# Kernel optimization log

Hardware: AMD Instinct MI355X
Metric: run time of the kernel (lower is better)

The kernel has to match this reference:

```python
import jax, jax.numpy as jnp
import numpy as np

B = 1 << 21          # shading points per batch
U_RES, CH = 400, 8   # spatial plane
A_RES, ACH = 50, 50 and 8  # placeholder, real consts below
A_RES, ACH = 50, 8   # angular planes (h/d)
HID = 32
IN_CH = CH + 2 * ACH  # 24


def _bilerp_clamp(tex, uv):
    # Bilinear interp, both axes clamped (U-plane). tex: (H,W,C), uv: (B,2) in [0,1]
    H, W, _ = tex.shape
    u = jnp.clip(uv[:, 0], 0.0, 1.0) * (W - 1)
    v = jnp.clip(uv[:, 1], 0.0, 1.0) * (H - 1)
    x0 = jnp.floor(u).astype(jnp.int32)
    x1 = jnp.clip(x0 + 1, 0, W - 1)
    y0 = jnp.floor(v).astype(jnp.int32)
    y1 = jnp.clip(y0 + 1, 0, H - 1)
    ur = (u - x0.astype(u.dtype))[:, None]
    vr = (v - y0.astype(v.dtype))[:, None]
    p00 = tex[y0, x0]; p10 = tex[y0, x1]; p01 = tex[y1, x0]; p11 = tex[y1, x1]
    return ((1 - ur) * (1 - vr) * p00 + ur * (1 - vr) * p10
            + (1 - ur) * vr * p01 + ur * vr * p11)


def _bilerp_wrap_u(tex, uv):
    # Bilinear interp wrapping the u (phi) axis, clamping v (H/D planes).
    H, W, _ = tex.shape
    u = (uv[:, 0] % 1.0) * W
    v = jnp.clip(uv[:, 1], 0.0, 1.0) * (H - 1)
    x0f = jnp.floor(u)
    x0 = x0f.astype(jnp.int32) % W
    x1 = (x0 + 1) % W
    y0 = jnp.floor(v).astype(jnp.int32)
    y1 = jnp.clip(y0 + 1, 0, H - 1)
    ur = (u - x0f)[:, None]
    vr = (v - y0.astype(v.dtype))[:, None]
    p00 = tex[y0, x0]; p10 = tex[y0, x1]; p01 = tex[y1, x0]; p11 = tex[y1, x1]
    return ((1 - ur) * (1 - vr) * p00 + ur * (1 - vr) * p10
            + (1 - ur) * vr * p01 + ur * vr * p11)


def setup_inputs() -> dict:
    key = jax.random.key(0)
    ks = jax.random.split(key, 8)
    x = jax.random.uniform(ks[0], (B, 6), dtype=jnp.float32)
    u_plane = 0.01 * jax.random.normal(ks[1], (U_RES, U_RES, CH), dtype=jnp.float32)
    h_plane = 0.01 * jax.random.normal(ks[2], (A_RES, A_RES, ACH), dtype=jnp.float32)
    d_plane = 0.01 * jax.random.normal(ks[3], (A_RES, A_RES, ACH), dtype=jnp.float32)
    def lin_w(k, fout, fin):  # torch nn.Linear default init (kaiming-uniform-ish)
        lim = 1.0 / np.sqrt(fin)
        return jax.random.uniform(k, (fout, fin), jnp.float32, -lim, lim)
    W0 = lin_w(ks[4], HID, IN_CH)
    W1 = lin_w(ks[5], HID, HID)
    W2 = lin_w(ks[6], HID, HID)
    W3 = lin_w(ks[7], 3, HID)
    return {"x": x, "u_plane": u_plane, "h_plane": h_plane, "d_plane": d_plane,
            "W0": W0, "W1": W1, "W2": W2, "W3": W3}


def reference(x, u_plane, h_plane, d_plane, W0, W1, W2, W3):
    # Split and reorder: H/D planes receive (u=phi, v=theta)
    uv = x[:, 0:2]
    h_uv = jnp.stack((x[:, 3], x[:, 2]), axis=1)
    d_uv = jnp.stack((x[:, 5], x[:, 4]), axis=1)
    fU = _bilerp_clamp(u_plane, uv)       # (B, CH)
    fH = _bilerp_wrap_u(h_plane, h_uv)    # (B, ACH)
    fD = _bilerp_wrap_u(d_plane, d_uv)    # (B, ACH)
    feat = jnp.concatenate([fU, fH, fD], axis=1)  # (B, 24)
    # Quant mode 'off' -> QLinear is a plain bias-free matmul with W^T
    h = jax.nn.relu(feat @ W0.T)
    h = jax.nn.relu(h @ W1.T)
    h = jax.nn.relu(h @ W2.T)
    return h @ W3.T  # (B, 3)
```

## Files before the change

kernel.cpp:

```cpp
#include <hip/hip_runtime.h>

typedef _Float16 half4 __attribute__((ext_vector_type(4)));
typedef _Float16 half8 __attribute__((ext_vector_type(8)));
typedef float floatx4 __attribute__((ext_vector_type(4)));

#define U_RESV 400
#define A_RESV 50

#define UHALVES (U_RESV * U_RESV * 8)
#define AHALVES (A_RESV * A_RESV * 8)
#define WOFF    (UHALVES + 2 * AHALVES)
#define W0OFF   0
#define W1OFF   896
#define W2OFF   2048
#define W3OFF   3200
#define WTOT    3776

__device__ __forceinline__ float clamp01(float x) { return fminf(fmaxf(x, 0.0f), 1.0f); }

__device__ __forceinline__ floatx4 mfma16(half4 a, half4 b, floatx4 c) {
    return __builtin_amdgcn_mfma_f32_16x16x16f16(a, b, c, 0, 0, 0);
}
__device__ __forceinline__ half4 zero4() {
    half4 h; h[0] = h[1] = h[2] = h[3] = (_Float16)0.f; return h;
}
__device__ __forceinline__ half4 relu4(half4 v) {
#if __has_builtin(__builtin_elementwise_max)
    return __builtin_elementwise_max(v, zero4());
#else
    half4 r;
#pragma unroll
    for (int i = 0; i < 4; ++i) r[i] = v[i] > (_Float16)0.f ? v[i] : (_Float16)0.f;
    return r;
#endif
}

__device__ __forceinline__ void cvt_chunk(const float* __restrict__ src,
                                          _Float16* __restrict__ dst, int i) {
    float4 a = *(const float4*)(src + (size_t)i * 8);
    float4 b = *(const float4*)(src + (size_t)i * 8 + 4);
    half8 h;
    h[0] = (_Float16)a.x; h[1] = (_Float16)a.y; h[2] = (_Float16)a.z; h[3] = (_Float16)a.w;
    h[4] = (_Float16)b.x; h[5] = (_Float16)b.y; h[6] = (_Float16)b.z; h[7] = (_Float16)b.w;
    *(half8*)(dst + (size_t)i * 8) = h;
}

__device__ __forceinline__ void wblob_fill(const float* __restrict__ W0,
                                           const float* __restrict__ W1,
                                           const float* __restrict__ W2,
                                           const float* __restrict__ W3,
                                           _Float16* __restrict__ w, int tid, int nthr) {
    for (int i = tid; i < WTOT; i += nthr) {
        float v;
        if (i < W1OFF) {
            int r = i / 28, c = i - r * 28;
            v = (c < 24) ? W0[r * 24 + c] : 0.f;
        } else if (i < W2OFF) {
            int j = i - W1OFF, r = j / 36, c = j - r * 36;
            v = (c < 32) ? W1[r * 32 + c] : 0.f;
        } else if (i < W3OFF) {
            int j = i - W2OFF, r = j / 36, c = j - r * 36;
            v = (c < 32) ? W2[r * 32 + c] : 0.f;
        } else {
            int j = i - W3OFF, r = j / 36, c = j - r * 36;
            v = (r < 3 && c < 32) ? W3[r * 32 + c] : 0.f;
        }
        w[i] = (_Float16)v;
    }
}

__global__ __launch_bounds__(256) void pconv_kernel(
    const float* __restrict__ u_plane, const float* __restrict__ h_plane,
    const float* __restrict__ d_plane, const float* __restrict__ W0,
    const float* __restrict__ W1, const float* __restrict__ W2,
    const float* __restrict__ W3, _Float16* __restrict__ dst) {
    const int gid = blockIdx.x * 256 + threadIdx.x;
    const int gsz = gridDim.x * 256;
    for (int i = gid; i < UHALVES / 8; i += gsz) cvt_chunk(u_plane, dst, i);
    for (int i = gid; i < AHALVES / 8; i += gsz) cvt_chunk(h_plane, dst + UHALVES, i);
    for (int i = gid; i < AHALVES / 8; i += gsz) cvt_chunk(d_plane, dst + UHALVES + AHALVES, i);
    if (blockIdx.x == 0) wblob_fill(W0, W1, W2, W3, dst + WOFF, threadIdx.x, 256);
}

__global__ __launch_bounds__(256) void wprep_kernel(
    const float* __restrict__ W0, const float* __restrict__ W1,
    const float* __restrict__ W2, const float* __restrict__ W3,
    _Float16* __restrict__ wdst) {
    wblob_fill(W0, W1, W2, W3, wdst, threadIdx.x, 256);
}


template <bool F16P>
__global__ __launch_bounds__(512, 2) void tpmlp_kernel(
    const float* __restrict__ x,
    const void* __restrict__ u_tex,
    const void* __restrict__ h_tex,
    const void* __restrict__ d_tex,
    const _Float16* __restrict__ wsw,
    float* __restrict__ out) {
    const int tid  = threadIdx.x;
    const int lane = tid & 63;
    const int wv   = tid >> 6;
    const int q    = lane >> 4;
    const int c15  = lane & 15;

    __shared__ __align__(16) _Float16 fl[512 * 28];
    __shared__ __align__(16) _Float16 wl[WTOT];

    const size_t P = (size_t)blockIdx.x * 512 + tid;
    const float2* xp = (const float2*)(x + P * 6);
    float2 p01v = xp[0], p23v = xp[1], p45v = xp[2];

    uint4 w_a;
    if (tid < 472) w_a = ((const uint4*)wsw)[tid];

    int oU0, oU1, oU2, oU3;  float uw00, uw10, uw01, uw11;
    {
        float u = clamp01(p01v.x) * (float)(U_RESV - 1);
        float v = clamp01(p01v.y) * (float)(U_RESV - 1);
        float x0f = floorf(u), y0f = floorf(v);
        int x0 = (int)x0f, y0 = (int)y0f;
        int x1 = min(x0 + 1, U_RESV - 1), y1 = min(y0 + 1, U_RESV - 1);
        float ur = u - x0f, vr = v - y0f;
        uw00 = (1.0f - ur) * (1.0f - vr); uw10 = ur * (1.0f - vr);
        uw01 = (1.0f - ur) * vr;          uw11 = ur * vr;
        oU0 = (y0 * U_RESV + x0) * 8;
        oU1 = (y0 * U_RESV + x1) * 8;
        oU2 = (y1 * U_RESV + x0) * 8;
        oU3 = (y1 * U_RESV + x1) * 8;
    }
    int oH0, oH1, oH2, oH3;  float hw00, hw10, hw01, hw11;
    {
        float uu = p23v.y, vv = p23v.x;
        float uf = uu - floorf(uu);
        float u = uf * (float)A_RESV;
        float v = clamp01(vv) * (float)(A_RESV - 1);
        float x0f = floorf(u), y0f = floorf(v);
        int x0 = (int)x0f;
        int x1 = x0 + 1; if (x1 == A_RESV) x1 = 0;
        int y0 = (int)y0f;
        int y1 = min(y0 + 1, A_RESV - 1);
        float ur = u - x0f, vr = v - y0f;
        hw00 = (1.0f - ur) * (1.0f - vr); hw10 = ur * (1.0f - vr);
        hw01 = (1.0f - ur) * vr;          hw11 = ur * vr;
        oH0 = (y0 * A_RESV + x0) * 8;
        oH1 = (y0 * A_RESV + x1) * 8;
        oH2 = (y1 * A_RESV + x0) * 8;
        oH3 = (y1 * A_RESV + x1) * 8;
    }
    int oD0, oD1, oD2, oD3;  float dw00, dw10, dw01, dw11;
    {
        float uu = p45v.y, vv = p45v.x;
        float uf = uu - floorf(uu);
        float u = uf * (float)A_RESV;
        float v = clamp01(vv) * (float)(A_RESV - 1);
        float x0f = floorf(u), y0f = floorf(v);
        int x0 = (int)x0f;
        int x1 = x0 + 1; if (x1 == A_RESV) x1 = 0;
        int y0 = (int)y0f;
        int y1 = min(y0 + 1, A_RESV - 1);
        float ur = u - x0f, vr = v - y0f;
        dw00 = (1.0f - ur) * (1.0f - vr); dw10 = ur * (1.0f - vr);
        dw01 = (1.0f - ur) * vr;          dw11 = ur * vr;
        oD0 = (y0 * A_RESV + x0) * 8;
        oD1 = (y0 * A_RESV + x1) * 8;
        oD2 = (y1 * A_RESV + x0) * 8;
        oD3 = (y1 * A_RESV + x1) * 8;
    }

    half8 gU0, gU1, gU2, gU3, gH0, gH1, gH2, gH3, gD0, gD1, gD2, gD3;
    float4 sU0, sU1, sU2, sU3, sH0, sH1, sH2, sH3, sD0, sD1, sD2, sD3;
    float4 rU0, rU1, rU2, rU3, rH0, rH1, rH2, rH3, rD0, rD1, rD2, rD3;
    if constexpr (F16P) {
        const _Float16* up = (const _Float16*)u_tex;
        const _Float16* hp = (const _Float16*)h_tex;
        const _Float16* dp = (const _Float16*)d_tex;
        gU0 = *(const half8*)(up + oU0);
        gU1 = *(const half8*)(up + oU1);
        gU2 = *(const half8*)(up + oU2);
        gU3 = *(const half8*)(up + oU3);
        gH0 = *(const half8*)(hp + oH0);
        gH1 = *(const half8*)(hp + oH1);
        gH2 = *(const half8*)(hp + oH2);
        gH3 = *(const half8*)(hp + oH3);
        gD0 = *(const half8*)(dp + oD0);
        gD1 = *(const half8*)(dp + oD1);
        gD2 = *(const half8*)(dp + oD2);
        gD3 = *(const half8*)(dp + oD3);
    } else {
        const float* up = (const float*)u_tex;
        const float* hp = (const float*)h_tex;
        const float* dp = (const float*)d_tex;
        sU0 = *(const float4*)(up + oU0); rU0 = *(const float4*)(up + oU0 + 4);
        sU1 = *(const float4*)(up + oU1); rU1 = *(const float4*)(up + oU1 + 4);
        sU2 = *(const float4*)(up + oU2); rU2 = *(const float4*)(up + oU2 + 4);
        sU3 = *(const float4*)(up + oU3); rU3 = *(const float4*)(up + oU3 + 4);
        sH0 = *(const float4*)(hp + oH0); rH0 = *(const float4*)(hp + oH0 + 4);
        sH1 = *(const float4*)(hp + oH1); rH1 = *(const float4*)(hp + oH1 + 4);
        sH2 = *(const float4*)(hp + oH2); rH2 = *(const float4*)(hp + oH2 + 4);
        sH3 = *(const float4*)(hp + oH3); rH3 = *(const float4*)(hp + oH3 + 4);
        sD0 = *(const float4*)(dp + oD0); rD0 = *(const float4*)(dp + oD0 + 4);
        sD1 = *(const float4*)(dp + oD1); rD1 = *(const float4*)(dp + oD1 + 4);
        sD2 = *(const float4*)(dp + oD2); rD2 = *(const float4*)(dp + oD2 + 4);
        sD3 = *(const float4*)(dp + oD3); rD3 = *(const float4*)(dp + oD3 + 4);
    }
    __builtin_amdgcn_sched_barrier(0);

    if (tid < 472) ((uint4*)wl)[tid] = w_a;
    asm volatile("s_waitcnt lgkmcnt(0)" ::: "memory");
    __builtin_amdgcn_s_barrier();

    float fU[8], fH[8], fD[8];
    if constexpr (F16P) {
#pragma unroll
        for (int i = 0; i < 8; ++i) {
            float r = (float)gU0[i] * uw00;
            r = fmaf((float)gU1[i], uw10, r);
            r = fmaf((float)gU2[i], uw01, r);
            r = fmaf((float)gU3[i], uw11, r);
            fU[i] = r;
        }
#pragma unroll
        for (int i = 0; i < 8; ++i) {
            float r = (float)gH0[i] * hw00;
            r = fmaf((float)gH1[i], hw10, r);
            r = fmaf((float)gH2[i], hw01, r);
            r = fmaf((float)gH3[i], hw11, r);
            fH[i] = r;
        }
#pragma unroll
        for (int i = 0; i < 8; ++i) {
            float r = (float)gD0[i] * dw00;
            r = fmaf((float)gD1[i], dw10, r);
            r = fmaf((float)gD2[i], dw01, r);
            r = fmaf((float)gD3[i], dw11, r);
            fD[i] = r;
        }
    } else {
        const float* a;
        const float* b;
        const float* c;
        const float* d;
#pragma unroll
        for (int i = 0; i < 8; ++i) {
            a = i < 4 ? (const float*)&sU0 : (const float*)&rU0;
            b = i < 4 ? (const float*)&sU1 : (const float*)&rU1;
            c = i < 4 ? (const float*)&sU2 : (const float*)&rU2;
            d = i < 4 ? (const float*)&sU3 : (const float*)&rU3;
            int k = i & 3;
            float r = a[k] * uw00;
            r = fmaf(b[k], uw10, r);
            r = fmaf(c[k], uw01, r);
            r = fmaf(d[k], uw11, r);
            fU[i] = r;
        }
#pragma unroll
        for (int i = 0; i < 8; ++i) {
            a = i < 4 ? (const float*)&sH0 : (const float*)&rH0;
            b = i < 4 ? (const float*)&sH1 : (const float*)&rH1;
            c = i < 4 ? (const float*)&sH2 : (const float*)&rH2;
            d = i < 4 ? (const float*)&sH3 : (const float*)&rH3;
            int k = i & 3;
            float r = a[k] * hw00;
            r = fmaf(b[k], hw10, r);
            r = fmaf(c[k], hw01, r);
            r = fmaf(d[k], hw11, r);
            fH[i] = r;
        }
#pragma unroll
        for (int i = 0; i < 8; ++i) {
            a = i < 4 ? (const float*)&sD0 : (const float*)&rD0;
            b = i < 4 ? (const float*)&sD1 : (const float*)&rD1;
            c = i < 4 ? (const float*)&sD2 : (const float*)&rD2;
            d = i < 4 ? (const float*)&sD3 : (const float*)&rD3;
            int k = i & 3;
            float r = a[k] * dw00;
            r = fmaf(b[k], dw10, r);
            r = fmaf(c[k], dw01, r);
            r = fmaf(d[k], dw11, r);
            fD[i] = r;
        }
    }

    {
        _Float16* row = fl + tid * 28;
        half8 hU, hH, hD;
#pragma unroll
        for (int i = 0; i < 8; ++i) {
            hU[i] = (_Float16)fU[i];
            hH[i] = (_Float16)fH[i];
            hD[i] = (_Float16)fD[i];
        }
        *(half8*)(row)      = hU;
        *(half8*)(row + 8)  = hH;
        *(half8*)(row + 16) = hD;
    }
    asm volatile("s_waitcnt lgkmcnt(0)" ::: "memory");
    __builtin_amdgcn_sched_barrier(0);

    floatx4 zf; zf[0] = 0.f; zf[1] = 0.f; zf[2] = 0.f; zf[3] = 0.f;
    const _Float16* wb = fl + (size_t)wv * 64 * 28;
    const _Float16* w0l = wl + W0OFF;
    const _Float16* w1l = wl + W1OFF;
    const _Float16* w2l = wl + W2OFF;
    const _Float16* w3l = wl + W3OFF;

    half4 b0[4], b1[4];
#pragma unroll
    for (int j = 0; j < 4; ++j) {
        const _Float16* r = wb + (size_t)(j * 16 + c15) * 28;
        b0[j] = *(const half4*)(r + q * 4);
        b1[j] = (q < 2) ? *(const half4*)(r + 16 + q * 4) : zero4();
    }

    floatx4 cc[2][4];
#pragma unroll
    for (int m = 0; m < 2; ++m) {
        half4 a0 = *(const half4*)(w0l + (size_t)(16 * m + c15) * 28 + q * 4);
        half4 a1 = (q < 2) ? *(const half4*)(w0l + (size_t)(16 * m + c15) * 28 + 16 + q * 4) : zero4();
#pragma unroll
        for (int j = 0; j < 4; ++j)
            cc[m][j] = mfma16(a1, b1[j], mfma16(a0, b0[j], zf));
    }
#pragma unroll
    for (int j = 0; j < 4; ++j) {
#pragma unroll
        for (int e = 0; e < 4; ++e) {
            b0[j][e] = (_Float16)cc[0][j][e];
            b1[j][e] = (_Float16)cc[1][j][e];
        }
        b0[j] = relu4(b0[j]);
        b1[j] = relu4(b1[j]);
    }

#pragma unroll
    for (int m = 0; m < 2; ++m) {
        half4 a0 = *(const half4*)(w1l + (size_t)(16 * m + c15) * 36 + q * 4);
        half4 a1 = *(const half4*)(w1l + (size_t)(16 * m + c15) * 36 + 16 + q * 4);
#pragma unroll
        for (int j = 0; j < 4; ++j)
            cc[m][j] = mfma16(a1, b1[j], mfma16(a0, b0[j], zf));
    }
#pragma unroll
    for (int j = 0; j < 4; ++j) {
#pragma unroll
        for (int e = 0; e < 4; ++e) {
            b0[j][e] = (_Float16)cc[0][j][e];
            b1[j][e] = (_Float16)cc[1][j][e];
        }
        b0[j] = relu4(b0[j]);
        b1[j] = relu4(b1[j]);
    }

#pragma unroll
    for (int m = 0; m < 2; ++m) {
        half4 a0 = *(const half4*)(w2l + (size_t)(16 * m + c15) * 36 + q * 4);
        half4 a1 = *(const half4*)(w2l + (size_t)(16 * m + c15) * 36 + 16 + q * 4);
#pragma unroll
        for (int j = 0; j < 4; ++j)
            cc[m][j] = mfma16(a1, b1[j], mfma16(a0, b0[j], zf));
    }
#pragma unroll
    for (int j = 0; j < 4; ++j) {
#pragma unroll
        for (int e = 0; e < 4; ++e) {
            b0[j][e] = (_Float16)cc[0][j][e];
            b1[j][e] = (_Float16)cc[1][j][e];
        }
        b0[j] = relu4(b0[j]);
        b1[j] = relu4(b1[j]);
    }

    floatx4 c3[4];
    {
        half4 a0 = *(const half4*)(w3l + (size_t)c15 * 36 + q * 4);
        half4 a1 = *(const half4*)(w3l + (size_t)c15 * 36 + 16 + q * 4);
#pragma unroll
        for (int j = 0; j < 4; ++j)
            c3[j] = mfma16(a1, b1[j], mfma16(a0, b0[j], zf));
    }

    if (lane < 16) {
        const size_t base = (size_t)blockIdx.x * 512 + (size_t)wv * 64;
#pragma unroll
        for (int j = 0; j < 4; ++j) {
            size_t p = base + (size_t)j * 16 + lane;
            float* o = out + p * 3;
            o[0] = c3[j][0];
            o[1] = c3[j][1];
            o[2] = c3[j][2];
        }
    }
}

extern "C" void kernel_launch(void* const* d_in, const int* in_sizes, int n_in,
                              void* d_out, int out_size, void* d_ws, size_t ws_size,
                              hipStream_t stream) {
    const float* x       = (const float*)d_in[0];
    const float* u_plane = (const float*)d_in[1];
    const float* h_plane = (const float*)d_in[2];
    const float* d_plane = (const float*)d_in[3];
    const float* W0      = (const float*)d_in[4];
    const float* W1      = (const float*)d_in[5];
    const float* W2      = (const float*)d_in[6];
    const float* W3      = (const float*)d_in[7];
    float* out = (float*)d_out;
    _Float16* wsw = (_Float16*)d_ws;

    int n = in_sizes[0] / 6;
    int grid = n / 512;

    const size_t need = ((size_t)WOFF + WTOT) * 2;
    if (ws_size >= need) {
        pconv_kernel<<<648, 256, 0, stream>>>(u_plane, h_plane, d_plane,
                                              W0, W1, W2, W3, wsw);
        tpmlp_kernel<true><<<grid, 512, 0, stream>>>(
            x, (const void*)wsw, (const void*)(wsw + UHALVES),
            (const void*)(wsw + UHALVES + AHALVES), wsw + WOFF, out);
    } else {
        wprep_kernel<<<1, 256, 0, stream>>>(W0, W1, W2, W3, wsw);
        tpmlp_kernel<false><<<grid, 512, 0, stream>>>(
            x, (const void*)u_plane, (const void*)h_plane, (const void*)d_plane,
            wsw, out);
    }
}
```

Before: 72.68 us.

## Software-pipeline texture gathers across multiple point tiles per block

```diff
diff --git a/kernel.cpp b/kernel.cpp
--- a/kernel.cpp
+++ b/kernel.cpp
@@ -89,13 +89,63 @@
     wblob_fill(W0, W1, W2, W3, wdst, threadIdx.x, 256);
 }
 
-
-template <bool F16P>
-__global__ __launch_bounds__(512, 2) void tpmlp_kernel(
+struct GA { int o0, o1, o2, o3; float w00, w10, w01, w11; };
+
+__device__ __forceinline__ GA mkU(float ux, float uy) {
+    GA g;
+    float u = clamp01(ux) * (float)(U_RESV - 1);
+    float v = clamp01(uy) * (float)(U_RESV - 1);
+    float x0f = floorf(u), y0f = floorf(v);
+    int x0 = (int)x0f, y0 = (int)y0f;
+    int x1 = min(x0 + 1, U_RESV - 1), y1 = min(y0 + 1, U_RESV - 1);
+    float ur = u - x0f, vr = v - y0f;
+    g.w00 = (1.0f - ur) * (1.0f - vr); g.w10 = ur * (1.0f - vr);
+    g.w01 = (1.0f - ur) * vr;          g.w11 = ur * vr;
+    g.o0 = (y0 * U_RESV + x0) * 8;
+    g.o1 = (y0 * U_RESV + x1) * 8;
+    g.o2 = (y1 * U_RESV + x0) * 8;
+    g.o3 = (y1 * U_RESV + x1) * 8;
+    return g;
+}
+__device__ __forceinline__ GA mkA(float uu, float vv) {
+    GA g;
+    float uf = uu - floorf(uu);
+    float u = uf * (float)A_RESV;
+    float v = clamp01(vv) * (float)(A_RESV - 1);
+    float x0f = floorf(u), y0f = floorf(v);
+    int x0 = (int)x0f;
+    int x1 = x0 + 1; if (x1 == A_RESV) x1 = 0;
+    int y0 = (int)y0f;
+    int y1 = min(y0 + 1, A_RESV - 1);
+    float ur = u - x0f, vr = v - y0f;
+    g.w00 = (1.0f - ur) * (1.0f - vr); g.w10 = ur * (1.0f - vr);
+    g.w01 = (1.0f - ur) * vr;          g.w11 = ur * vr;
+    g.o0 = (y0 * A_RESV + x0) * 8;
+    g.o1 = (y0 * A_RESV + x1) * 8;
+    g.o2 = (y1 * A_RESV + x0) * 8;
+    g.o3 = (y1 * A_RESV + x1) * 8;
+    return g;
+}
+
+__device__ __forceinline__ void blend8(half8 a, half8 b, half8 c, half8 d,
+                                       const GA& g, float* f) {
+#pragma unroll
+    for (int i = 0; i < 8; ++i) {
+        float r = (float)a[i] * g.w00;
+        r = fmaf((float)b[i], g.w10, r);
+        r = fmaf((float)c[i], g.w01, r);
+        r = fmaf((float)d[i], g.w11, r);
+        f[i] = r;
+    }
+}
+
+
+template <int K>
+__global__ __launch_bounds__(256, 2) void tpmlp_pipe(
     const float* __restrict__ x,
-    const void* __restrict__ u_tex,
-    const void* __restrict__ h_tex,
-    const void* __restrict__ d_tex,
+    const _Float16* __restrict__ up,
+    const _Float16* __restrict__ hp,
+    const _Float16* __restrict__ dp,
     const _Float16* __restrict__ wsw,
     float* __restrict__ out) {
     const int tid  = threadIdx.x;
@@ -104,6 +154,210 @@
     const int q    = lane >> 4;
     const int c15  = lane & 15;
 
+    __shared__ __align__(16) _Float16 fl[256 * 28];
+    __shared__ __align__(16) _Float16 wl[WTOT];
+
+    {
+        const uint4* src = (const uint4*)wsw;
+        uint4 a = src[tid];
+        uint4 b;
+        if (tid < 472 - 256) b = src[256 + tid];
+        uint4* dst = (uint4*)wl;
+        dst[tid] = a;
+        if (tid < 472 - 256) dst[256 + tid] = b;
+    }
+    __syncthreads();
+
+    const _Float16* wb  = fl + (size_t)wv * 64 * 28;
+    const _Float16* w0l = wl + W0OFF;
+    const _Float16* w1l = wl + W1OFF;
+    const _Float16* w2l = wl + W2OFF;
+    const _Float16* w3l = wl + W3OFF;
+    const size_t blkbase = (size_t)blockIdx.x * (256 * K);
+
+    auto xload = [&](int it, float2& a, float2& b, float2& c) {
+        const float2* p = (const float2*)(x + (blkbase + (size_t)it * 256 + tid) * 6);
+        a = p[0]; b = p[1]; c = p[2];
+    };
+
+    float2 c01, c23, c45;
+    float2 n01, n23, n45;
+    xload(0, c01, c23, c45);
+    if (K > 1) xload(1, n01, n23, n45);
+
+    GA gU = mkU(c01.x, c01.y);
+    GA gH = mkA(c23.y, c23.x);
+    GA gD = mkA(c45.y, c45.x);
+    half8 tU0 = *(const half8*)(up + gU.o0);
+    half8 tU1 = *(const half8*)(up + gU.o1);
+    half8 tU2 = *(const half8*)(up + gU.o2);
+    half8 tU3 = *(const half8*)(up + gU.o3);
+    half8 tH0 = *(const half8*)(hp + gH.o0);
+    half8 tH1 = *(const half8*)(hp + gH.o1);
+    half8 tH2 = *(const half8*)(hp + gH.o2);
+    half8 tH3 = *(const half8*)(hp + gH.o3);
+    half8 tD0 = *(const half8*)(dp + gD.o0);
+    half8 tD1 = *(const half8*)(dp + gD.o1);
+    half8 tD2 = *(const half8*)(dp + gD.o2);
+    half8 tD3 = *(const half8*)(dp + gD.o3);
+    __builtin_amdgcn_sched_barrier(0);
+
+#pragma unroll
+    for (int it = 0; it < K; ++it) {
+        GA pU, pH, pD;
+        half8 mU0, mU1, mU2, mU3, mH0, mH1, mH2, mH3, mD0, mD1, mD2, mD3;
+        float2 f01 = n01, f23 = n23, f45 = n45;
+        if (it + 2 < K) xload(it + 2, n01, n23, n45);
+        if (it + 1 < K) {
+            pU = mkU(f01.x, f01.y);
+            pH = mkA(f23.y, f23.x);
+            pD = mkA(f45.y, f45.x);
+            mU0 = *(const half8*)(up + pU.o0);
+            mU1 = *(const half8*)(up + pU.o1);
+            mU2 = *(const half8*)(up + pU.o2);
+            mU3 = *(const half8*)(up + pU.o3);
+            mH0 = *(const half8*)(hp + pH.o0);
+            mH1 = *(const half8*)(hp + pH.o1);
+            mH2 = *(const half8*)(hp + pH.o2);
+            mH3 = *(const half8*)(hp + pH.o3);
+            mD0 = *(const half8*)(dp + pD.o0);
+            mD1 = *(const half8*)(dp + pD.o1);
+            mD2 = *(const half8*)(dp + pD.o2);
+            mD3 = *(const half8*)(dp + pD.o3);
+            __builtin_amdgcn_sched_barrier(0);
+        }
+
+        float fU[8], fH[8], fD[8];
+        blend8(tU0, tU1, tU2, tU3, gU, fU);
+        blend8(tH0, tH1, tH2, tH3, gH, fH);
+        blend8(tD0, tD1, tD2, tD3, gD, fD);
+
+        {
+            _Float16* row = fl + tid * 28;
+            half8 hU, hH, hD;
+#pragma unroll
+            for (int i = 0; i < 8; ++i) {
+                hU[i] = (_Float16)fU[i];
+                hH[i] = (_Float16)fH[i];
+                hD[i] = (_Float16)fD[i];
+            }
+            *(half8*)(row)      = hU;
+            *(half8*)(row + 8)  = hH;
+            *(half8*)(row + 16) = hD;
+        }
+        asm volatile("s_waitcnt lgkmcnt(0)" ::: "memory");
+        __builtin_amdgcn_sched_barrier(0);
+
+        floatx4 zf; zf[0] = 0.f; zf[1] = 0.f; zf[2] = 0.f; zf[3] = 0.f;
+        half4 b0[4], b1[4];
+#pragma unroll
+        for (int j = 0; j < 4; ++j) {
+            const _Float16* r = wb + (size_t)(j * 16 + c15) * 28;
+            b0[j] = *(const half4*)(r + q * 4);
+            b1[j] = (q < 2) ? *(const half4*)(r + 16 + q * 4) : zero4();
+        }
+
+        floatx4 cc[2][4];
+#pragma unroll
+        for (int m = 0; m < 2; ++m) {
+            half4 a0 = *(const half4*)(w0l + (size_t)(16 * m + c15) * 28 + q * 4);
+            half4 a1 = (q < 2) ? *(const half4*)(w0l + (size_t)(16 * m + c15) * 28 + 16 + q * 4) : zero4();
+#pragma unroll
+            for (int j = 0; j < 4; ++j)
+                cc[m][j] = mfma16(a1, b1[j], mfma16(a0, b0[j], zf));
+        }
+#pragma unroll
+        for (int j = 0; j < 4; ++j) {
+#pragma unroll
+            for (int e = 0; e < 4; ++e) {
+                b0[j][e] = (_Float16)cc[0][j][e];
+                b1[j][e] = (_Float16)cc[1][j][e];
+            }
+            b0[j] = relu4(b0[j]);
+            b1[j] = relu4(b1[j]);
+        }
+
+#pragma unroll
+        for (int m = 0; m < 2; ++m) {
+            half4 a0 = *(const half4*)(w1l + (size_t)(16 * m + c15) * 36 + q * 4);
+            half4 a1 = *(const half4*)(w1l + (size_t)(16 * m + c15) * 36 + 16 + q * 4);
+#pragma unroll
+            for (int j = 0; j < 4; ++j)
+                cc[m][j] = mfma16(a1, b1[j], mfma16(a0, b0[j], zf));
+        }
+#pragma unroll
+        for (int j = 0; j < 4; ++j) {
+#pragma unroll
+            for (int e = 0; e < 4; ++e) {
+                b0[j][e] = (_Float16)cc[0][j][e];
+                b1[j][e] = (_Float16)cc[1][j][e];
+            }
+            b0[j] = relu4(b0[j]);
+            b1[j] = relu4(b1[j]);
+        }
+
+#pragma unroll
+        for (int m = 0; m < 2; ++m) {
+            half4 a0 = *(const half4*)(w2l + (size_t)(16 * m + c15) * 36 + q * 4);
+            half4 a1 = *(const half4*)(w2l + (size_t)(16 * m + c15) * 36 + 16 + q * 4);
+#pragma unroll
+            for (int j = 0; j < 4; ++j)
+                cc[m][j] = mfma16(a1, b1[j], mfma16(a0, b0[j], zf));
+        }
+#pragma unroll
+        for (int j = 0; j < 4; ++j) {
+#pragma unroll
+            for (int e = 0; e < 4; ++e) {
+                b0[j][e] = (_Float16)cc[0][j][e];
+                b1[j][e] = (_Float16)cc[1][j][e];
+            }
+            b0[j] = relu4(b0[j]);
+            b1[j] = relu4(b1[j]);
+        }
+
+        floatx4 c3[4];
+        {
+            half4 a0 = *(const half4*)(w3l + (size_t)c15 * 36 + q * 4);
+            half4 a1 = *(const half4*)(w3l + (size_t)c15 * 36 + 16 + q * 4);
+#pragma unroll
+            for (int j = 0; j < 4; ++j)
+                c3[j] = mfma16(a1, b1[j], mfma16(a0, b0[j], zf));
+        }
+
+        if (lane < 16) {
+            const size_t base = blkbase + (size_t)it * 256 + (size_t)wv * 64;
+#pragma unroll
+            for (int j = 0; j < 4; ++j) {
+                size_t p = base + (size_t)j * 16 + lane;
+                float* o = out + p * 3;
+                o[0] = c3[j][0];
+                o[1] = c3[j][1];
+                o[2] = c3[j][2];
+            }
+        }
+
+        if (it + 1 < K) {
+            gU = pU; gH = pH; gD = pD;
+            tU0 = mU0; tU1 = mU1; tU2 = mU2; tU3 = mU3;
+            tH0 = mH0; tH1 = mH1; tH2 = mH2; tH3 = mH3;
+            tD0 = mD0; tD1 = mD1; tD2 = mD2; tD3 = mD3;
+        }
+    }
+}
+
+__global__ __launch_bounds__(512, 2) void tpmlp_f32(
+    const float* __restrict__ x,
+    const float* __restrict__ up,
+    const float* __restrict__ hp,
+    const float* __restrict__ dp,
+    const _Float16* __restrict__ wsw,
+    float* __restrict__ out) {
+    const int tid  = threadIdx.x;
+    const int lane = tid & 63;
+    const int wv   = tid >> 6;
+    const int q    = lane >> 4;
+    const int c15  = lane & 15;
+
     __shared__ __align__(16) _Float16 fl[512 * 28];
     __shared__ __align__(16) _Float16 wl[WTOT];
 
@@ -114,96 +368,22 @@
     uint4 w_a;
     if (tid < 472) w_a = ((const uint4*)wsw)[tid];
 
-    int oU0, oU1, oU2, oU3;  float uw00, uw10, uw01, uw11;
-    {
-        float u = clamp01(p01v.x) * (float)(U_RESV - 1);
-        float v = clamp01(p01v.y) * (float)(U_RESV - 1);
-        float x0f = floorf(u), y0f = floorf(v);
-        int x0 = (int)x0f, y0 = (int)y0f;
-        int x1 = min(x0 + 1, U_RESV - 1), y1 = min(y0 + 1, U_RESV - 1);
-        float ur = u - x0f, vr = v - y0f;
-        uw00 = (1.0f - ur) * (1.0f - vr); uw10 = ur * (1.0f - vr);
-        uw01 = (1.0f - ur) * vr;          uw11 = ur * vr;
-        oU0 = (y0 * U_RESV + x0) * 8;
-        oU1 = (y0 * U_RESV + x1) * 8;
-        oU2 = (y1 * U_RESV + x0) * 8;
-        oU3 = (y1 * U_RESV + x1) * 8;
-    }
-    int oH0, oH1, oH2, oH3;  float hw00, hw10, hw01, hw11;
-    {
-        float uu = p23v.y, vv = p23v.x;
-        float uf = uu - floorf(uu);
-        float u = uf * (float)A_RESV;
-        float v = clamp01(vv) * (float)(A_RESV - 1);
-        float x0f = floorf(u), y0f = floorf(v);
-        int x0 = (int)x0f;
-        int x1 = x0 + 1; if (x1 == A_RESV) x1 = 0;
-        int y0 = (int)y0f;
-        int y1 = min(y0 + 1, A_RESV - 1);
-        float ur = u - x0f, vr = v - y0f;
-        hw00 = (1.0f - ur) * (1.0f - vr); hw10 = ur * (1.0f - vr);
-        hw01 = (1.0f - ur) * vr;          hw11 = ur * vr;
-        oH0 = (y0 * A_RESV + x0) * 8;
-        oH1 = (y0 * A_RESV + x1) * 8;
-        oH2 = (y1 * A_RESV + x0) * 8;
-        oH3 = (y1 * A_RESV + x1) * 8;
-    }
-    int oD0, oD1, oD2, oD3;  float dw00, dw10, dw01, dw11;
-    {
-        float uu = p45v.y, vv = p45v.x;
-        float uf = uu - floorf(uu);
-        float u = uf * (float)A_RESV;
-        float v = clamp01(vv) * (float)(A_RESV - 1);
-        float x0f = floorf(u), y0f = floorf(v);
-        int x0 = (int)x0f;
-        int x1 = x0 + 1; if (x1 == A_RESV) x1 = 0;
-        int y0 = (int)y0f;
-        int y1 = min(y0 + 1, A_RESV - 1);
-        float ur = u - x0f, vr = v - y0f;
-        dw00 = (1.0f - ur) * (1.0f - vr); dw10 = ur * (1.0f - vr);
-        dw01 = (1.0f - ur) * vr;          dw11 = ur * vr;
-        oD0 = (y0 * A_RESV + x0) * 8;
-        oD1 = (y0 * A_RESV + x1) * 8;
-        oD2 = (y1 * A_RESV + x0) * 8;
-        oD3 = (y1 * A_RESV + x1) * 8;
-    }
-
-    half8 gU0, gU1, gU2, gU3, gH0, gH1, gH2, gH3, gD0, gD1, gD2, gD3;
-    float4 sU0, sU1, sU2, sU3, sH0, sH1, sH2, sH3, sD0, sD1, sD2, sD3;
-    float4 rU0, rU1, rU2, rU3, rH0, rH1, rH2, rH3, rD0, rD1, rD2, rD3;
-    if constexpr (F16P) {
-        const _Float16* up = (const _Float16*)u_tex;
-        const _Float16* hp = (const _Float16*)h_tex;
-        const _Float16* dp = (const _Float16*)d_tex;
-        gU0 = *(const half8*)(up + oU0);
-        gU1 = *(const half8*)(up + oU1);
-        gU2 = *(const half8*)(up + oU2);
-        gU3 = *(const half8*)(up + oU3);
-        gH0 = *(const half8*)(hp + oH0);
-        gH1 = *(const half8*)(hp + oH1);
-        gH2 = *(const half8*)(hp + oH2);
-        gH3 = *(const half8*)(hp + oH3);
-        gD0 = *(const half8*)(dp + oD0);
-        gD1 = *(const half8*)(dp + oD1);
-        gD2 = *(const half8*)(dp + oD2);
-        gD3 = *(const half8*)(dp + oD3);
-    } else {
-        const float* up = (const float*)u_tex;
-        const float* hp = (const float*)h_tex;
-        const float* dp = (const float*)d_tex;
-        sU0 = *(const float4*)(up + oU0); rU0 = *(const float4*)(up + oU0 + 4);
-        sU1 = *(const float4*)(up + oU1); rU1 = *(const float4*)(up + oU1 + 4);
-        sU2 = *(const float4*)(up + oU2); rU2 = *(const float4*)(up + oU2 + 4);
-        sU3 = *(const float4*)(up + oU3); rU3 = *(const float4*)(up + oU3 + 4);
-        sH0 = *(const float4*)(hp + oH0); rH0 = *(const float4*)(hp + oH0 + 4);
-        sH1 = *(const float4*)(hp + oH1); rH1 = *(const float4*)(hp + oH1 + 4);
-        sH2 = *(const float4*)(hp + oH2); rH2 = *(const float4*)(hp + oH2 + 4);
-        sH3 = *(const float4*)(hp + oH3); rH3 = *(const float4*)(hp + oH3 + 4);
-        sD0 = *(const float4*)(dp + oD0); rD0 = *(const float4*)(dp + oD0 + 4);
-        sD1 = *(const float4*)(dp + oD1); rD1 = *(const float4*)(dp + oD1 + 4);
-        sD2 = *(const float4*)(dp + oD2); rD2 = *(const float4*)(dp + oD2 + 4);
-        sD3 = *(const float4*)(dp + oD3); rD3 = *(const float4*)(dp + oD3 + 4);
-    }
+    GA gU = mkU(p01v.x, p01v.y);
+    GA gH = mkA(p23v.y, p23v.x);
+    GA gD = mkA(p45v.y, p45v.x);
+
+    float4 sU0 = *(const float4*)(up + gU.o0); float4 rU0 = *(const float4*)(up + gU.o0 + 4);
+    float4 sU1 = *(const float4*)(up + gU.o1); float4 rU1 = *(const float4*)(up + gU.o1 + 4);
+    float4 sU2 = *(const float4*)(up + gU.o2); float4 rU2 = *(const float4*)(up + gU.o2 + 4);
+    float4 sU3 = *(const float4*)(up + gU.o3); float4 rU3 = *(const float4*)(up + gU.o3 + 4);
+    float4 sH0 = *(const float4*)(hp + gH.o0); float4 rH0 = *(const float4*)(hp + gH.o0 + 4);
+    float4 sH1 = *(const float4*)(hp + gH.o1); float4 rH1 = *(const float4*)(hp + gH.o1 + 4);
+    float4 sH2 = *(const float4*)(hp + gH.o2); float4 rH2 = *(const float4*)(hp + gH.o2 + 4);
+    float4 sH3 = *(const float4*)(hp + gH.o3); float4 rH3 = *(const float4*)(hp + gH.o3 + 4);
+    float4 sD0 = *(const float4*)(dp + gD.o0); float4 rD0 = *(const float4*)(dp + gD.o0 + 4);
+    float4 sD1 = *(const float4*)(dp + gD.o1); float4 rD1 = *(const float4*)(dp + gD.o1 + 4);
+    float4 sD2 = *(const float4*)(dp + gD.o2); float4 rD2 = *(const float4*)(dp + gD.o2 + 4);
+    float4 sD3 = *(const float4*)(dp + gD.o3); float4 rD3 = *(const float4*)(dp + gD.o3 + 4);
     __builtin_amdgcn_sched_barrier(0);
 
     if (tid < 472) ((uint4*)wl)[tid] = w_a;
@@ -211,75 +391,44 @@
     __builtin_amdgcn_s_barrier();
 
     float fU[8], fH[8], fD[8];
-    if constexpr (F16P) {
-#pragma unroll
-        for (int i = 0; i < 8; ++i) {
-            float r = (float)gU0[i] * uw00;
-            r = fmaf((float)gU1[i], uw10, r);
-            r = fmaf((float)gU2[i], uw01, r);
-            r = fmaf((float)gU3[i], uw11, r);
-            fU[i] = r;
-        }
-#pragma unroll
-        for (int i = 0; i < 8; ++i) {
-            float r = (float)gH0[i] * hw00;
-            r = fmaf((float)gH1[i], hw10, r);
-            r = fmaf((float)gH2[i], hw01, r);
-            r = fmaf((float)gH3[i], hw11, r);
-            fH[i] = r;
-        }
-#pragma unroll
-        for (int i = 0; i < 8; ++i) {
-            float r = (float)gD0[i] * dw00;
-            r = fmaf((float)gD1[i], dw10, r);
-            r = fmaf((float)gD2[i], dw01, r);
-            r = fmaf((float)gD3[i], dw11, r);
-            fD[i] = r;
-        }
-    } else {
-        const float* a;
-        const float* b;
-        const float* c;
-        const float* d;
-#pragma unroll
-        for (int i = 0; i < 8; ++i) {
-            a = i < 4 ? (const float*)&sU0 : (const float*)&rU0;
-            b = i < 4 ? (const float*)&sU1 : (const float*)&rU1;
-            c = i < 4 ? (const float*)&sU2 : (const float*)&rU2;
-            d = i < 4 ? (const float*)&sU3 : (const float*)&rU3;
-            int k = i & 3;
-            float r = a[k] * uw00;
-            r = fmaf(b[k], uw10, r);
-            r = fmaf(c[k], uw01, r);
-            r = fmaf(d[k], uw11, r);
-            fU[i] = r;
-        }
-#pragma unroll
-        for (int i = 0; i < 8; ++i) {
-            a = i < 4 ? (const float*)&sH0 : (const float*)&rH0;
-            b = i < 4 ? (const float*)&sH1 : (const float*)&rH1;
-            c = i < 4 ? (const float*)&sH2 : (const float*)&rH2;
-            d = i < 4 ? (const float*)&sH3 : (const float*)&rH3;
-            int k = i & 3;
-            float r = a[k] * hw00;
-            r = fmaf(b[k], hw10, r);
-            r = fmaf(c[k], hw01, r);
-            r = fmaf(d[k], hw11, r);
-            fH[i] = r;
-        }
-#pragma unroll
-        for (int i = 0; i < 8; ++i) {
-            a = i < 4 ? (const float*)&sD0 : (const float*)&rD0;
-            b = i < 4 ? (const float*)&sD1 : (const float*)&rD1;
-            c = i < 4 ? (const float*)&sD2 : (const float*)&rD2;
-            d = i < 4 ? (const float*)&sD3 : (const float*)&rD3;
-            int k = i & 3;
-            float r = a[k] * dw00;
-            r = fmaf(b[k], dw10, r);
-            r = fmaf(c[k], dw01, r);
-            r = fmaf(d[k], dw11, r);
-            fD[i] = r;
-        }
+#pragma unroll
+    for (int i = 0; i < 8; ++i) {
+        const float* a = i < 4 ? (const float*)&sU0 : (const float*)&rU0;
+        const float* b = i < 4 ? (const float*)&sU1 : (const float*)&rU1;
+        const float* c = i < 4 ? (const float*)&sU2 : (const float*)&rU2;
+        const float* d = i < 4 ? (const float*)&sU3 : (const float*)&rU3;
+        int k = i & 3;
+        float r = a[k] * gU.w00;
+        r = fmaf(b[k], gU.w10, r);
+        r = fmaf(c[k], gU.w01, r);
+        r = fmaf(d[k], gU.w11, r);
+        fU[i] = r;
+    }
+#pragma unroll
+    for (int i = 0; i < 8; ++i) {
+        const float* a = i < 4 ? (const float*)&sH0 : (const float*)&rH0;
+        const float* b = i < 4 ? (const float*)&sH1 : (const float*)&rH1;
+        const float* c = i < 4 ? (const float*)&sH2 : (const float*)&rH2;
+        const float* d = i < 4 ? (const float*)&sH3 : (const float*)&rH3;
+        int k = i & 3;
+        float r = a[k] * gH.w00;
+        r = fmaf(b[k], gH.w10, r);
+        r = fmaf(c[k], gH.w01, r);
+        r = fmaf(d[k], gH.w11, r);
+        fH[i] = r;
+    }
+#pragma unroll
+    for (int i = 0; i < 8; ++i) {
+        const float* a = i < 4 ? (const float*)&sD0 : (const float*)&rD0;
+        const float* b = i < 4 ? (const float*)&sD1 : (const float*)&rD1;
+        const float* c = i < 4 ? (const float*)&sD2 : (const float*)&rD2;
+        const float* d = i < 4 ? (const float*)&sD3 : (const float*)&rD3;
+        int k = i & 3;
+        float r = a[k] * gD.w00;
+        r = fmaf(b[k], gD.w10, r);
+        r = fmaf(c[k], gD.w01, r);
+        r = fmaf(d[k], gD.w11, r);
+        fD[i] = r;
     }
 
     {
@@ -332,7 +481,6 @@
         b0[j] = relu4(b0[j]);
         b1[j] = relu4(b1[j]);
     }
-
 #pragma unroll
     for (int m = 0; m < 2; ++m) {
         half4 a0 = *(const half4*)(w1l + (size_t)(16 * m + c15) * 36 + q * 4);
@@ -351,7 +499,6 @@
         b0[j] = relu4(b0[j]);
         b1[j] = relu4(b1[j]);
     }
-
 #pragma unroll
     for (int m = 0; m < 2; ++m) {
         half4 a0 = *(const half4*)(w2l + (size_t)(16 * m + c15) * 36 + q * 4);
@@ -408,19 +555,18 @@
     _Float16* wsw = (_Float16*)d_ws;
 
     int n = in_sizes[0] / 6;
-    int grid = n / 512;
+    constexpr int K = 8;
 
     const size_t need = ((size_t)WOFF + WTOT) * 2;
     if (ws_size >= need) {
         pconv_kernel<<<648, 256, 0, stream>>>(u_plane, h_plane, d_plane,
                                               W0, W1, W2, W3, wsw);
-        tpmlp_kernel<true><<<grid, 512, 0, stream>>>(
-            x, (const void*)wsw, (const void*)(wsw + UHALVES),
-            (const void*)(wsw + UHALVES + AHALVES), wsw + WOFF, out);
+        int grid = n / (256 * K);
+        tpmlp_pipe<K><<<grid, 256, 0, stream>>>(
+            x, wsw, wsw + UHALVES, wsw + UHALVES + AHALVES, wsw + WOFF, out);
     } else {
         wprep_kernel<<<1, 256, 0, stream>>>(W0, W1, W2, W3, wsw);
-        tpmlp_kernel<false><<<grid, 512, 0, stream>>>(
-            x, (const void*)u_plane, (const void*)h_plane, (const void*)d_plane,
-            wsw, out);
-    }
-}
+        tpmlp_f32<<<n / 512, 512, 0, stream>>>(
+            x, u_plane, h_plane, d_plane, wsw, out);
+    }
+}
```

Result: slower. 75.52 us (+3.9%).
